# Kernel tuning notes

Hardware: AMD Instinct MI355X
Metric: run time of the kernel (lower is better)

## Reference

```python
import jax, jax.numpy as jnp
import numpy as np

C = 256       # in_channels
A = 6         # act_dim
B = 10000     # number of graphs (batch)
N = B * A     # total nodes
E = 960000    # number of edges
H = 32        # hidden_size


def setup_inputs() -> dict:
    key = jax.random.key(0)
    ks = jax.random.split(key, 20)
    s = 1.0 / np.sqrt(C)
    inp = {
        "state": jax.random.normal(ks[0], (N, C), jnp.float32),
        "edge_index": jax.random.randint(ks[1], (2, E), 0, N, jnp.int32),
        "action": jax.random.uniform(ks[2], (B, A), jnp.float32),
    }
    # GCNConv params (weight [C,C], bias [C]); conv4/conv5 exist but are unused by forward
    for i in range(5):
        inp[f"W{i+1}"] = jax.random.normal(ks[3 + i], (C, C), jnp.float32) * s
        inp[f"b{i+1}"] = jnp.zeros((C,), jnp.float32)
    D1 = 6 * C + 1
    inp["lin1_w"] = jax.random.normal(ks[10], (D1, H), jnp.float32) / np.sqrt(D1)
    inp["lin1_b"] = jnp.zeros((H,), jnp.float32)
    inp["lin2_w"] = jax.random.normal(ks[11], (H, H), jnp.float32) / np.sqrt(H)
    inp["lin2_b"] = jnp.zeros((H,), jnp.float32)
    inp["lin3_w"] = jax.random.normal(ks[12], (H, 1), jnp.float32) / np.sqrt(H)
    inp["lin3_b"] = jnp.zeros((1,), jnp.float32)
    return inp


def _gcn(x, W, b, src, dst, dinv):
    # PyG GCNConv: xW, then D^{-1/2}(A+I)D^{-1/2} aggregation, then bias.
    xw = x @ W                                    # [N, C]
    norm = dinv[src] * dinv[dst]                  # [E]
    agg = jax.ops.segment_sum(xw[src] * norm[:, None], dst, num_segments=N)
    agg = agg + xw * (dinv * dinv)[:, None]       # self-loop term
    return agg + b


def reference(state, edge_index, action,
              W1, b1, W2, b2, W3, b3, W4, b4, W5, b5,
              lin1_w, lin1_b, lin2_w, lin2_b, lin3_w, lin3_b):
    src, dst = edge_index[0], edge_index[1]
    # degree of A + I, computed at destination nodes (gcn_norm with self-loops)
    deg = jax.ops.segment_sum(jnp.ones((E,), state.dtype), dst, num_segments=N) + 1.0
    dinv = jax.lax.rsqrt(deg)

    o1 = jax.nn.relu(_gcn(state, W1, b1, src, dst, dinv))
    o2 = jax.nn.relu(_gcn(o1, W2, b2, src, dst, dinv))
    o3 = jax.nn.relu(_gcn(o2, W3, b3, src, dst, dinv))
    # NOTE: original forward reuses conv3 for layers 4 and 5 (replicated faithfully)
    o4 = jax.nn.relu(_gcn(o3, W3, b3, src, dst, dinv))
    o5 = jax.nn.relu(_gcn(o4, W3, b3, src, dst, dinv))

    r = lambda t: t.reshape(-1, A, C)             # [B, A, C]
    concat = jnp.concatenate(
        [r(o1), r(o2), r(o3), r(o4), r(o5), r(state), action[..., None]], axis=-1)
    x = jax.nn.relu(concat @ lin1_w + lin1_b)     # [B, A, H]
    x = jax.nn.relu(x @ lin2_w + lin2_b)
    x = jnp.sum(x, axis=1)                        # readout over act_dim
    x = (x @ lin3_w + lin3_b).squeeze(-1)         # [B]
    return x
```

## Files before the change

### kernel.cpp

```cpp
#include <hip/hip_runtime.h>
#include <hip/hip_fp16.h>

#define NNODES 60000
#define NEDGES 960000
#define NGRAPH 10000

struct __align__(16) H8 { __half2 h[4]; };
struct __align__(8)  H4 { __half2 h[2]; };

typedef _Float16 f16x8 __attribute__((ext_vector_type(8)));
typedef float f32x4 __attribute__((ext_vector_type(4)));


__global__ void count_deg_k(const int* __restrict__ ei, int* __restrict__ deg) {
  int e = blockIdx.x * blockDim.x + threadIdx.x;
  atomicAdd(&deg[ei[NEDGES + e]], 1);
}

__global__ void scan1_k(const int* __restrict__ deg, int* __restrict__ rs,
                        int* __restrict__ bsum, float* __restrict__ dinv) {
  __shared__ int s[256];
  int tid = threadIdx.x;
  int i = blockIdx.x * 256 + tid;
  int v = (i < NNODES) ? deg[i] : 0;
  if (i < NNODES) dinv[i] = rsqrtf((float)v + 1.0f);
  int x = v;
  s[tid] = x; __syncthreads();
  #pragma unroll
  for (int off = 1; off < 256; off <<= 1) {
    int t = (tid >= off) ? s[tid - off] : 0;
    __syncthreads();
    x += t; s[tid] = x; __syncthreads();
  }
  if (i < NNODES) rs[i] = x - v;
  if (tid == 255) bsum[blockIdx.x] = x;
}

__global__ void scan2_k(int* __restrict__ bsum, int nb) {
  __shared__ int s[256];
  int tid = threadIdx.x;
  int v = (tid < nb) ? bsum[tid] : 0;
  int x = v; s[tid] = x; __syncthreads();
  #pragma unroll
  for (int off = 1; off < 256; off <<= 1) {
    int t = (tid >= off) ? s[tid - off] : 0;
    __syncthreads();
    x += t; s[tid] = x; __syncthreads();
  }
  if (tid < nb) bsum[tid] = x - v;
}

__global__ void scan3_k(int* __restrict__ rs, const int* __restrict__ bsum) {
  int i = blockIdx.x * 256 + threadIdx.x;
  if (i < NNODES) rs[i] += bsum[blockIdx.x];
  if (i == 0) rs[NNODES] = NEDGES;
}

__global__ void scatter_k(const int* __restrict__ ei, const int* __restrict__ rs,
                          int* __restrict__ cursor, unsigned short* __restrict__ csr) {
  int e = blockIdx.x * blockDim.x + threadIdx.x;
  int s = ei[e], d = ei[NEDGES + e];
  int pos = rs[d] + atomicAdd(&cursor[d], 1);
  csr[pos] = (unsigned short)s;
}


__launch_bounds__(256)
__global__ void f2hskern_k(const float* __restrict__ state, const float* __restrict__ lw,
                           __half* __restrict__ stateh, float* __restrict__ part) {
  __shared__ float os[32][256];
  int tid = threadIdx.x;
  int n0 = blockIdx.x * 32;
  #pragma unroll
  for (int l = 0; l < 4; ++l) {
    int f = tid + l * 256;
    int row = f >> 5, c8 = (f & 31) * 8;
    const float* src = state + (size_t)(n0 + row) * 256 + c8;
    float4 u = *reinterpret_cast<const float4*>(src);
    float4 v = *reinterpret_cast<const float4*>(src + 4);
    float* dst = &os[row][c8];
    dst[0] = u.x; dst[1] = u.y; dst[2] = u.z; dst[3] = u.w;
    dst[4] = v.x; dst[5] = v.y; dst[6] = v.z; dst[7] = v.w;
    H8 o;
    o.h[0].x = __float2half_rn(u.x); o.h[0].y = __float2half_rn(u.y);
    o.h[1].x = __float2half_rn(u.z); o.h[1].y = __float2half_rn(u.w);
    o.h[2].x = __float2half_rn(v.x); o.h[2].y = __float2half_rn(v.y);
    o.h[3].x = __float2half_rn(v.z); o.h[3].y = __float2half_rn(v.w);
    *reinterpret_cast<H8*>(stateh + (size_t)(n0 + row) * 256 + c8) = o;
  }
  __syncthreads();
  int dim = tid & 31, rblk = tid >> 5;
  float a0 = 0.f, a1 = 0.f, a2 = 0.f, a3 = 0.f;
  #pragma unroll 8
  for (int k = 0; k < 256; ++k) {
    float w = lw[k * 32 + dim];
    a0 += os[rblk * 4 + 0][k] * w;
    a1 += os[rblk * 4 + 1][k] * w;
    a2 += os[rblk * 4 + 2][k] * w;
    a3 += os[rblk * 4 + 3][k] * w;
  }
  int base = (n0 + rblk * 4) * 32 + dim;
  part[base] = a0;
  part[base + 32] = a1;
  part[base + 64] = a2;
  part[base + 96] = a3;
}


__global__ void wconv3_k(const float* __restrict__ W1, const float* __restrict__ W2,
                         const float* __restrict__ W3, __half* __restrict__ T1,
                         __half* __restrict__ T2, __half* __restrict__ T3) {
  int n = blockIdx.x & 255, which = blockIdx.x >> 8, k = threadIdx.x;
  const float* W = which == 0 ? W1 : (which == 1 ? W2 : W3);
  __half* T = which == 0 ? T1 : (which == 1 ? T2 : T3);
  T[n * 256 + k] = __float2half_rn(W[k * 256 + n]);
}

__global__ void wconvL_k(const float* __restrict__ l1w, __half* __restrict__ lwhT) {
  int dimg = blockIdx.x;
  int l = dimg >> 5, dim = dimg & 31, k = threadIdx.x;
  lwhT[(size_t)dimg * 256 + k] = __float2half_rn(l1w[((size_t)l * 256 + k) * 32 + dim]);
}


#define LDA 264

__launch_bounds__(256, 3)
__global__ void gemm_mfma_k(const __half* __restrict__ Xh, const __half* __restrict__ WhT,
                            const float* __restrict__ dinv, __half* __restrict__ Y,
                            const __half* __restrict__ lwhT, float* __restrict__ part) {
  __shared__ _Float16 As[64][LDA];
  const int tid = threadIdx.x;
  const int m0 = blockIdx.x * 64;
  const int lane = tid & 63;
  const int wid = tid >> 6;
  const int wr = wid >> 1, wc = wid & 1;
  const int li = lane & 15, lg = lane >> 4;

  #pragma unroll
  for (int l = 0; l < 8; ++l) {
    int f = l * 256 + tid;
    int row = f >> 5, c8 = (f & 31) * 8;
    int gr = m0 + row; if (gr >= NNODES) gr = NNODES - 1;
    *reinterpret_cast<H8*>(&As[row][c8]) =
        *reinterpret_cast<const H8*>(Xh + (size_t)gr * 256 + c8);
  }
  __syncthreads();

  f32x4 acc[2][8];
  #pragma unroll
  for (int i = 0; i < 2; ++i)
    #pragma unroll
    for (int j = 0; j < 8; ++j) acc[i][j] = (f32x4){0.f, 0.f, 0.f, 0.f};

  #pragma unroll
  for (int k0 = 0; k0 < 256; k0 += 32) {
    f16x8 a0 = *reinterpret_cast<const f16x8*>(&As[wr * 32 + li][k0 + lg * 8]);
    f16x8 a1 = *reinterpret_cast<const f16x8*>(&As[wr * 32 + 16 + li][k0 + lg * 8]);
    f16x8 b[8];
    #pragma unroll
    for (int cf = 0; cf < 8; ++cf)
      b[cf] = *reinterpret_cast<const f16x8*>(
          WhT + (size_t)(wc * 128 + cf * 16 + li) * 256 + k0 + lg * 8);
    #pragma unroll
    for (int cf = 0; cf < 8; ++cf) {
      acc[0][cf] = __builtin_amdgcn_mfma_f32_16x16x32_f16(b[cf], a0, acc[0][cf], 0, 0, 0);
      acc[1][cf] = __builtin_amdgcn_mfma_f32_16x16x32_f16(b[cf], a1, acc[1][cf], 0, 0, 0);
    }
  }

  #pragma unroll
  for (int rf = 0; rf < 2; ++rf) {
    int r = m0 + wr * 32 + rf * 16 + li;
    if (r < NNODES) {
      float dv = dinv[r];
      #pragma unroll
      for (int cf = 0; cf < 8; ++cf) {
        int n = wc * 128 + cf * 16 + lg * 4;
        H4 o;
        o.h[0].x = __float2half_rn(acc[rf][cf][0] * dv);
        o.h[0].y = __float2half_rn(acc[rf][cf][1] * dv);
        o.h[1].x = __float2half_rn(acc[rf][cf][2] * dv);
        o.h[1].y = __float2half_rn(acc[rf][cf][3] * dv);
        *reinterpret_cast<H4*>(Y + (size_t)r * 256 + n) = o;
      }
    }
  }

  if (lwhT != nullptr) {
    f32x4 pacc[2];
    pacc[0] = (f32x4){0.f, 0.f, 0.f, 0.f};
    pacc[1] = (f32x4){0.f, 0.f, 0.f, 0.f};
    #pragma unroll
    for (int k0 = 0; k0 < 256; k0 += 32) {
      f16x8 a = *reinterpret_cast<const f16x8*>(&As[wid * 16 + li][k0 + lg * 8]);
      f16x8 b0 = *reinterpret_cast<const f16x8*>(lwhT + (size_t)li * 256 + k0 + lg * 8);
      f16x8 b1 = *reinterpret_cast<const f16x8*>(lwhT + (size_t)(16 + li) * 256 + k0 + lg * 8);
      pacc[0] = __builtin_amdgcn_mfma_f32_16x16x32_f16(b0, a, pacc[0], 0, 0, 0);
      pacc[1] = __builtin_amdgcn_mfma_f32_16x16x32_f16(b1, a, pacc[1], 0, 0, 0);
    }
    int r = m0 + wid * 16 + li;
    if (r < NNODES) {
      #pragma unroll
      for (int cf = 0; cf < 2; ++cf) {
        float4 v;
        v.x = pacc[cf][0]; v.y = pacc[cf][1]; v.z = pacc[cf][2]; v.w = pacc[cf][3];
        *reinterpret_cast<float4*>(part + (size_t)r * 32 + cf * 16 + lg * 4) = v;
      }
    }
  }
}


__device__ inline void addH8(float* acc, const H8& v) {
  #pragma unroll
  for (int q = 0; q < 4; ++q) {
    acc[q * 2 + 0] += __low2float(v.h[q]);
    acc[q * 2 + 1] += __high2float(v.h[q]);
  }
}

__global__ void gather_k(const __half* __restrict__ ysh, const int* __restrict__ rs,
                         const unsigned short* __restrict__ csr, const float* __restrict__ dinv,
                         const float* __restrict__ bias, __half* __restrict__ out) {
  int tid = threadIdx.x;
  int lane = tid & 63;
  int wave = (blockIdx.x * blockDim.x + tid) >> 6;
  int d = wave * 2 + (lane >> 5);
  int c8 = (lane & 31) * 8;

  float acc[8];
  H8 self = *reinterpret_cast<const H8*>(ysh + (size_t)d * 256 + c8);
  #pragma unroll
  for (int q = 0; q < 4; ++q) {
    acc[q * 2 + 0] = __low2float(self.h[q]);
    acc[q * 2 + 1] = __high2float(self.h[q]);
  }

  int e = rs[d], end = rs[d + 1];
  for (; e + 3 < end; e += 4) {
    int s0 = csr[e], s1 = csr[e + 1], s2 = csr[e + 2], s3 = csr[e + 3];
    H8 v0 = *reinterpret_cast<const H8*>(ysh + (size_t)s0 * 256 + c8);
    H8 v1 = *reinterpret_cast<const H8*>(ysh + (size_t)s1 * 256 + c8);
    H8 v2 = *reinterpret_cast<const H8*>(ysh + (size_t)s2 * 256 + c8);
    H8 v3 = *reinterpret_cast<const H8*>(ysh + (size_t)s3 * 256 + c8);
    addH8(acc, v0);
    addH8(acc, v1);
    addH8(acc, v2);
    addH8(acc, v3);
  }
  for (; e < end; ++e) {
    int s0 = csr[e];
    H8 v0 = *reinterpret_cast<const H8*>(ysh + (size_t)s0 * 256 + c8);
    addH8(acc, v0);
  }

  float dv = dinv[d];
  float4 b0 = *reinterpret_cast<const float4*>(bias + c8);
  float4 b1 = *reinterpret_cast<const float4*>(bias + c8 + 4);
  float r0 = fmaxf(acc[0] * dv + b0.x, 0.f);
  float r1 = fmaxf(acc[1] * dv + b0.y, 0.f);
  float r2 = fmaxf(acc[2] * dv + b0.z, 0.f);
  float r3 = fmaxf(acc[3] * dv + b0.w, 0.f);
  float r4 = fmaxf(acc[4] * dv + b1.x, 0.f);
  float r5 = fmaxf(acc[5] * dv + b1.y, 0.f);
  float r6 = fmaxf(acc[6] * dv + b1.z, 0.f);
  float r7 = fmaxf(acc[7] * dv + b1.w, 0.f);
  H8 o;
  o.h[0].x = __float2half_rn(r0); o.h[0].y = __float2half_rn(r1);
  o.h[1].x = __float2half_rn(r2); o.h[1].y = __float2half_rn(r3);
  o.h[2].x = __float2half_rn(r4); o.h[2].y = __float2half_rn(r5);
  o.h[3].x = __float2half_rn(r6); o.h[3].y = __float2half_rn(r7);
  *reinterpret_cast<H8*>(out + (size_t)d * 256 + c8) = o;
}


__launch_bounds__(256)
__global__ void skern_k(const __half* __restrict__ in, const float* __restrict__ lw,
                        float* __restrict__ part) {
  __shared__ float os[32][256];
  int tid = threadIdx.x;
  int n0 = blockIdx.x * 32;
  #pragma unroll
  for (int l = 0; l < 4; ++l) {
    int f = tid + l * 256;
    int row = f >> 5, c8 = (f & 31) * 8;
    H8 v = *reinterpret_cast<const H8*>(in + (size_t)(n0 + row) * 256 + c8);
    float* dst = &os[row][c8];
    dst[0] = __low2float(v.h[0]); dst[1] = __high2float(v.h[0]);
    dst[2] = __low2float(v.h[1]); dst[3] = __high2float(v.h[1]);
    dst[4] = __low2float(v.h[2]); dst[5] = __high2float(v.h[2]);
    dst[6] = __low2float(v.h[3]); dst[7] = __high2float(v.h[3]);
  }
  __syncthreads();
  int dim = tid & 31, rblk = tid >> 5;
  float a0 = 0.f, a1 = 0.f, a2 = 0.f, a3 = 0.f;
  #pragma unroll 8
  for (int k = 0; k < 256; ++k) {
    float w = lw[k * 32 + dim];
    a0 += os[rblk * 4 + 0][k] * w;
    a1 += os[rblk * 4 + 1][k] * w;
    a2 += os[rblk * 4 + 2][k] * w;
    a3 += os[rblk * 4 + 3][k] * w;
  }
  int base = (n0 + rblk * 4) * 32 + dim;
  part[base] = a0;
  part[base + 32] = a1;
  part[base + 64] = a2;
  part[base + 96] = a3;
}


__launch_bounds__(192)
__global__ void mlpfinal_k(const float* __restrict__ p0, const float* __restrict__ p1,
                           const float* __restrict__ p2, const float* __restrict__ p3,
                           const float* __restrict__ p4, const float* __restrict__ p5,
                           const float* __restrict__ action, const float* __restrict__ l1wlast,
                           const float* __restrict__ l1b, const float* __restrict__ l2w,
                           const float* __restrict__ l2b, const float* __restrict__ l3w,
                           const float* __restrict__ l3b, float* __restrict__ out) {
  __shared__ float w2s[1024];
  __shared__ float h1s[6][33];
  __shared__ float red[3];
  int tid = threadIdx.x;
  for (int i = tid; i < 1024; i += 192) w2s[i] = l2w[i];
  int a = tid >> 5, dim = tid & 31;
  int n = blockIdx.x * 6 + a;
  int idx = n * 32 + dim;
  float h1 = l1b[dim] + action[n] * l1wlast[dim]
           + p0[idx] + p1[idx] + p2[idx] + p3[idx] + p4[idx] + p5[idx];
  h1s[a][dim] = fmaxf(h1, 0.f);
  __syncthreads();
  float acc = l2b[dim];
  #pragma unroll
  for (int k = 0; k < 32; ++k) acc += h1s[a][k] * w2s[k * 32 + dim];
  float v = fmaxf(acc, 0.f) * l3w[dim];
  #pragma unroll
  for (int off = 32; off; off >>= 1) v += __shfl_down(v, off, 64);
  int lane = tid & 63, wave = tid >> 6;
  if (lane == 0) red[wave] = v;
  __syncthreads();
  if (tid == 0) out[blockIdx.x] = red[0] + red[1] + red[2] + l3b[0];
}


extern "C" void kernel_launch(void* const* d_in, const int* in_sizes, int n_in,
                              void* d_out, int out_size, void* d_ws, size_t ws_size,
                              hipStream_t stream) {
  const float* state  = (const float*)d_in[0];
  const int*   ei     = (const int*)d_in[1];
  const float* action = (const float*)d_in[2];
  const float* W1 = (const float*)d_in[3];
  const float* b1 = (const float*)d_in[4];
  const float* W2 = (const float*)d_in[5];
  const float* b2 = (const float*)d_in[6];
  const float* W3 = (const float*)d_in[7];
  const float* b3 = (const float*)d_in[8];
  const float* l1w = (const float*)d_in[13];
  const float* l1b = (const float*)d_in[14];
  const float* l2w = (const float*)d_in[15];
  const float* l2b = (const float*)d_in[16];
  const float* l3w = (const float*)d_in[17];
  const float* l3b = (const float*)d_in[18];
  float* out = (float*)d_out;

  char* base = (char*)d_ws;
  size_t off = 0;
  auto carve = [&](size_t bytes) {
    char* q = base + off;
    off += (bytes + 255) & ~(size_t)255;
    return q;
  };
  __half* ysh    = (__half*)carve((size_t)NNODES * 256 * 2);
  __half* obufh  = (__half*)carve((size_t)NNODES * 256 * 2);
  __half* stateh = (__half*)carve((size_t)NNODES * 256 * 2);
  __half* whT1   = (__half*)carve(256 * 256 * 2);
  __half* whT2   = (__half*)carve(256 * 256 * 2);
  __half* whT3   = (__half*)carve(256 * 256 * 2);
  __half* lwhT   = (__half*)carve(5 * 32 * 256 * 2);
  float* parts[6];
  for (int i = 0; i < 6; ++i) parts[i] = (float*)carve((size_t)NNODES * 32 * 4);
  float* dinv  = (float*)carve(NNODES * 4);
  char*  zbase = (char*)carve(0);
  int*   deg   = (int*)carve(NNODES * 4);
  int*   cursor= (int*)carve(NNODES * 4);
  size_t zlen  = (size_t)((char*)carve(0) - zbase);
  int*   rs    = (int*)carve((NNODES + 1) * 4);
  unsigned short* csr = (unsigned short*)carve((size_t)NEDGES * 2);
  int*   bsum  = (int*)carve(256 * 4);

  hipMemsetAsync(zbase, 0, zlen, stream);

  f2hskern_k<<<NNODES / 32, 256, 0, stream>>>(state, l1w + 1280 * 32, stateh, parts[5]);
  wconv3_k<<<256 * 3, 256, 0, stream>>>(W1, W2, W3, whT1, whT2, whT3);
  wconvL_k<<<160, 256, 0, stream>>>(l1w, lwhT);

  count_deg_k<<<NEDGES / 256, 256, 0, stream>>>(ei, deg);
  int nb = (NNODES + 255) / 256;
  scan1_k<<<nb, 256, 0, stream>>>(deg, rs, bsum, dinv);
  scan2_k<<<1, 256, 0, stream>>>(bsum, nb);
  scan3_k<<<nb, 256, 0, stream>>>(rs, bsum);
  scatter_k<<<NEDGES / 256, 256, 0, stream>>>(ei, rs, cursor, csr);

  const __half* whTs[5] = {whT1, whT2, whT3, whT3, whT3};
  const float*  bs[5]   = {b1, b2, b3, b3, b3};
  const __half* in = stateh;
  int mblocks = (NNODES + 63) / 64;
  for (int layer = 0; layer < 5; ++layer) {
    const __half* plw = (layer == 0) ? nullptr : lwhT + (size_t)(layer - 1) * 32 * 256;
    float* ppart = (layer == 0) ? nullptr : parts[layer - 1];
    gemm_mfma_k<<<mblocks, 256, 0, stream>>>(in, whTs[layer], dinv, ysh, plw, ppart);
    gather_k<<<NNODES / 8, 256, 0, stream>>>(ysh, rs, csr, dinv, bs[layer], obufh);
    in = obufh;
  }
  skern_k<<<NNODES / 32, 256, 0, stream>>>(obufh, l1w + 1024 * 32, parts[4]);
  mlpfinal_k<<<NGRAPH, 192, 0, stream>>>(parts[0], parts[1], parts[2], parts[3], parts[4],
                                         parts[5], action, l1w + 1536 * 32, l1b, l2w, l2b,
                                         l3w, l3b, out);
}
```

Measured before the change: 766.1 us.

## Fuse neighbor gather into next-layer GEMM and fold fp32 state conversion into first GEMM

Each GCN layer's gather/aggregation now runs in the prologue of the next layer's MFMA GEMM kernel, writing the aggregated rows straight into shared memory instead of round-tripping through a global buffer. The first GEMM reads fp32 state directly and converts it in-kernel, which removes the separate conversion/state-partial kernel. The lin1 partial MFMA is interleaved into the main k-loop, and outputs are staged through LDS for coalesced stores, with ping-pong output buffers. In exchange, each 64-row block does its gather with only 8 rows per 32-lane group serially, which may expose more gather latency and reduce parallelism compared with the standalone gather kernel.

```diff
diff --git a/kernel.cpp b/kernel.cpp
--- a/kernel.cpp
+++ b/kernel.cpp
@@ -10,6 +10,8 @@
 
 typedef _Float16 f16x8 __attribute__((ext_vector_type(8)));
 typedef float f32x4 __attribute__((ext_vector_type(4)));
+
+#define LDA 264
 
 
 __global__ void count_deg_k(const int* __restrict__ ei, int* __restrict__ deg) {
@@ -65,48 +67,6 @@
 }
 
 
-__launch_bounds__(256)
-__global__ void f2hskern_k(const float* __restrict__ state, const float* __restrict__ lw,
-                           __half* __restrict__ stateh, float* __restrict__ part) {
-  __shared__ float os[32][256];
-  int tid = threadIdx.x;
-  int n0 = blockIdx.x * 32;
-  #pragma unroll
-  for (int l = 0; l < 4; ++l) {
-    int f = tid + l * 256;
-    int row = f >> 5, c8 = (f & 31) * 8;
-    const float* src = state + (size_t)(n0 + row) * 256 + c8;
-    float4 u = *reinterpret_cast<const float4*>(src);
-    float4 v = *reinterpret_cast<const float4*>(src + 4);
-    float* dst = &os[row][c8];
-    dst[0] = u.x; dst[1] = u.y; dst[2] = u.z; dst[3] = u.w;
-    dst[4] = v.x; dst[5] = v.y; dst[6] = v.z; dst[7] = v.w;
-    H8 o;
-    o.h[0].x = __float2half_rn(u.x); o.h[0].y = __float2half_rn(u.y);
-    o.h[1].x = __float2half_rn(u.z); o.h[1].y = __float2half_rn(u.w);
-    o.h[2].x = __float2half_rn(v.x); o.h[2].y = __float2half_rn(v.y);
-    o.h[3].x = __float2half_rn(v.z); o.h[3].y = __float2half_rn(v.w);
-    *reinterpret_cast<H8*>(stateh + (size_t)(n0 + row) * 256 + c8) = o;
-  }
-  __syncthreads();
-  int dim = tid & 31, rblk = tid >> 5;
-  float a0 = 0.f, a1 = 0.f, a2 = 0.f, a3 = 0.f;
-  #pragma unroll 8
-  for (int k = 0; k < 256; ++k) {
-    float w = lw[k * 32 + dim];
-    a0 += os[rblk * 4 + 0][k] * w;
-    a1 += os[rblk * 4 + 1][k] * w;
-    a2 += os[rblk * 4 + 2][k] * w;
-    a3 += os[rblk * 4 + 3][k] * w;
-  }
-  int base = (n0 + rblk * 4) * 32 + dim;
-  part[base] = a0;
-  part[base + 32] = a1;
-  part[base + 64] = a2;
-  part[base + 96] = a3;
-}
-
-
 __global__ void wconv3_k(const float* __restrict__ W1, const float* __restrict__ W2,
                          const float* __restrict__ W3, __half* __restrict__ T1,
                          __half* __restrict__ T2, __half* __restrict__ T3) {
@@ -123,92 +83,111 @@
 }
 
 
-#define LDA 264
-
-__launch_bounds__(256, 3)
-__global__ void gemm_mfma_k(const __half* __restrict__ Xh, const __half* __restrict__ WhT,
-                            const float* __restrict__ dinv, __half* __restrict__ Y,
-                            const __half* __restrict__ lwhT, float* __restrict__ part) {
-  __shared__ _Float16 As[64][LDA];
-  const int tid = threadIdx.x;
-  const int m0 = blockIdx.x * 64;
+__device__ __forceinline__ void gemm_body(
+    _Float16 (*As)[LDA], int m0, int tid,
+    const __half* __restrict__ WhT, const __half* __restrict__ lwhT,
+    const float* __restrict__ dinv, __half* __restrict__ Y,
+    float* __restrict__ part) {
   const int lane = tid & 63;
   const int wid = tid >> 6;
   const int wr = wid >> 1, wc = wid & 1;
   const int li = lane & 15, lg = lane >> 4;
 
-  #pragma unroll
-  for (int l = 0; l < 8; ++l) {
-    int f = l * 256 + tid;
-    int row = f >> 5, c8 = (f & 31) * 8;
-    int gr = m0 + row; if (gr >= NNODES) gr = NNODES - 1;
-    *reinterpret_cast<H8*>(&As[row][c8]) =
-        *reinterpret_cast<const H8*>(Xh + (size_t)gr * 256 + c8);
-  }
-  __syncthreads();
-
   f32x4 acc[2][8];
   #pragma unroll
   for (int i = 0; i < 2; ++i)
     #pragma unroll
     for (int j = 0; j < 8; ++j) acc[i][j] = (f32x4){0.f, 0.f, 0.f, 0.f};
+  f32x4 p0 = (f32x4){0.f, 0.f, 0.f, 0.f};
+  f32x4 p1 = (f32x4){0.f, 0.f, 0.f, 0.f};
 
   #pragma unroll
   for (int k0 = 0; k0 < 256; k0 += 32) {
     f16x8 a0 = *reinterpret_cast<const f16x8*>(&As[wr * 32 + li][k0 + lg * 8]);
     f16x8 a1 = *reinterpret_cast<const f16x8*>(&As[wr * 32 + 16 + li][k0 + lg * 8]);
+    f16x8 ap = *reinterpret_cast<const f16x8*>(&As[wid * 16 + li][k0 + lg * 8]);
     f16x8 b[8];
     #pragma unroll
     for (int cf = 0; cf < 8; ++cf)
       b[cf] = *reinterpret_cast<const f16x8*>(
           WhT + (size_t)(wc * 128 + cf * 16 + li) * 256 + k0 + lg * 8);
+    f16x8 bp0 = *reinterpret_cast<const f16x8*>(lwhT + (size_t)li * 256 + k0 + lg * 8);
+    f16x8 bp1 = *reinterpret_cast<const f16x8*>(lwhT + (size_t)(16 + li) * 256 + k0 + lg * 8);
     #pragma unroll
     for (int cf = 0; cf < 8; ++cf) {
       acc[0][cf] = __builtin_amdgcn_mfma_f32_16x16x32_f16(b[cf], a0, acc[0][cf], 0, 0, 0);
       acc[1][cf] = __builtin_amdgcn_mfma_f32_16x16x32_f16(b[cf], a1, acc[1][cf], 0, 0, 0);
     }
-  }
+    p0 = __builtin_amdgcn_mfma_f32_16x16x32_f16(bp0, ap, p0, 0, 0, 0);
+    p1 = __builtin_amdgcn_mfma_f32_16x16x32_f16(bp1, ap, p1, 0, 0, 0);
+  }
+
+  __syncthreads();
 
   #pragma unroll
   for (int rf = 0; rf < 2; ++rf) {
-    int r = m0 + wr * 32 + rf * 16 + li;
-    if (r < NNODES) {
-      float dv = dinv[r];
-      #pragma unroll
-      for (int cf = 0; cf < 8; ++cf) {
-        int n = wc * 128 + cf * 16 + lg * 4;
-        H4 o;
-        o.h[0].x = __float2half_rn(acc[rf][cf][0] * dv);
-        o.h[0].y = __float2half_rn(acc[rf][cf][1] * dv);
-        o.h[1].x = __float2half_rn(acc[rf][cf][2] * dv);
-        o.h[1].y = __float2half_rn(acc[rf][cf][3] * dv);
-        *reinterpret_cast<H4*>(Y + (size_t)r * 256 + n) = o;
-      }
+    int row = wr * 32 + rf * 16 + li;
+    int r = m0 + row;
+    float dv = (r < NNODES) ? dinv[r] : 0.f;
+    #pragma unroll
+    for (int cf = 0; cf < 8; ++cf) {
+      int col = wc * 128 + cf * 16 + lg * 4;
+      H4 o;
+      o.h[0].x = __float2half_rn(acc[rf][cf][0] * dv);
+      o.h[0].y = __float2half_rn(acc[rf][cf][1] * dv);
+      o.h[1].x = __float2half_rn(acc[rf][cf][2] * dv);
+      o.h[1].y = __float2half_rn(acc[rf][cf][3] * dv);
+      *reinterpret_cast<H4*>(&As[row][col]) = o;
     }
   }
 
-  if (lwhT != nullptr) {
-    f32x4 pacc[2];
-    pacc[0] = (f32x4){0.f, 0.f, 0.f, 0.f};
-    pacc[1] = (f32x4){0.f, 0.f, 0.f, 0.f};
-    #pragma unroll
-    for (int k0 = 0; k0 < 256; k0 += 32) {
-      f16x8 a = *reinterpret_cast<const f16x8*>(&As[wid * 16 + li][k0 + lg * 8]);
-      f16x8 b0 = *reinterpret_cast<const f16x8*>(lwhT + (size_t)li * 256 + k0 + lg * 8);
-      f16x8 b1 = *reinterpret_cast<const f16x8*>(lwhT + (size_t)(16 + li) * 256 + k0 + lg * 8);
-      pacc[0] = __builtin_amdgcn_mfma_f32_16x16x32_f16(b0, a, pacc[0], 0, 0, 0);
-      pacc[1] = __builtin_amdgcn_mfma_f32_16x16x32_f16(b1, a, pacc[1], 0, 0, 0);
-    }
-    int r = m0 + wid * 16 + li;
-    if (r < NNODES) {
-      #pragma unroll
-      for (int cf = 0; cf < 2; ++cf) {
-        float4 v;
-        v.x = pacc[cf][0]; v.y = pacc[cf][1]; v.z = pacc[cf][2]; v.w = pacc[cf][3];
-        *reinterpret_cast<float4*>(part + (size_t)r * 32 + cf * 16 + lg * 4) = v;
-      }
-    }
-  }
+  int pr = m0 + wid * 16 + li;
+  if (pr < NNODES) {
+    float4 v0, v1;
+    v0.x = p0[0]; v0.y = p0[1]; v0.z = p0[2]; v0.w = p0[3];
+    v1.x = p1[0]; v1.y = p1[1]; v1.z = p1[2]; v1.w = p1[3];
+    *reinterpret_cast<float4*>(part + (size_t)pr * 32 + lg * 4) = v0;
+    *reinterpret_cast<float4*>(part + (size_t)pr * 32 + 16 + lg * 4) = v1;
+  }
+
+  __syncthreads();
+
+  #pragma unroll
+  for (int l = 0; l < 8; ++l) {
+    int f = l * 256 + tid;
+    int row = f >> 5, c8 = (f & 31) * 8;
+    int gr = m0 + row;
+    if (gr < NNODES)
+      *reinterpret_cast<H8*>(Y + (size_t)gr * 256 + c8) =
+          *reinterpret_cast<const H8*>(&As[row][c8]);
+  }
+}
+
+
+__launch_bounds__(256, 3)
+__global__ void gemm0_k(const float* __restrict__ Xf, const __half* __restrict__ WhT,
+                        const float* __restrict__ dinv, __half* __restrict__ Y,
+                        const __half* __restrict__ lwhT, float* __restrict__ part) {
+  __shared__ _Float16 As[64][LDA];
+  const int tid = threadIdx.x;
+  const int m0 = blockIdx.x * 64;
+  #pragma unroll
+  for (int l = 0; l < 8; ++l) {
+    int f = l * 256 + tid;
+    int row = f >> 5, c8 = (f & 31) * 8;
+    int gr = m0 + row; if (gr >= NNODES) gr = NNODES - 1;
+    const float* src = Xf + (size_t)gr * 256 + c8;
+    float4 u = *reinterpret_cast<const float4*>(src);
+    float4 v = *reinterpret_cast<const float4*>(src + 4);
+    H8 o;
+    o.h[0].x = __float2half_rn(u.x); o.h[0].y = __float2half_rn(u.y);
+    o.h[1].x = __float2half_rn(u.z); o.h[1].y = __float2half_rn(u.w);
+    o.h[2].x = __float2half_rn(v.x); o.h[2].y = __float2half_rn(v.y);
+    o.h[3].x = __float2half_rn(v.z); o.h[3].y = __float2half_rn(v.w);
+    *reinterpret_cast<H8*>(&As[row][c8]) = o;
+  }
+  __syncthreads();
+  gemm_body(As, m0, tid, WhT, lwhT, dinv, Y, part);
 }
 
 
@@ -219,6 +198,72 @@
     acc[q * 2 + 1] += __high2float(v.h[q]);
   }
 }
+
+__launch_bounds__(256, 3)
+__global__ void ggemm_k(const __half* __restrict__ ysin, const int* __restrict__ rs,
+                        const unsigned short* __restrict__ csr,
+                        const float* __restrict__ dinv, const float* __restrict__ bias,
+                        const __half* __restrict__ WhT, const __half* __restrict__ lwhT,
+                        __half* __restrict__ Yout, float* __restrict__ part) {
+  __shared__ _Float16 As[64][LDA];
+  const int tid = threadIdx.x;
+  const int m0 = blockIdx.x * 64;
+  const int half = tid >> 5;
+  const int c8 = (tid & 31) * 8;
+
+  float4 b0 = *reinterpret_cast<const float4*>(bias + c8);
+  float4 b1 = *reinterpret_cast<const float4*>(bias + c8 + 4);
+
+  for (int i = 0; i < 8; ++i) {
+    int d = m0 + half * 8 + i;
+    int dc = (d < NNODES) ? d : NNODES - 1;
+
+    float acc[8];
+    H8 self = *reinterpret_cast<const H8*>(ysin + (size_t)dc * 256 + c8);
+    #pragma unroll
+    for (int q = 0; q < 4; ++q) {
+      acc[q * 2 + 0] = __low2float(self.h[q]);
+      acc[q * 2 + 1] = __high2float(self.h[q]);
+    }
+
+    int e = rs[dc], end = rs[dc + 1];
+    for (; e + 3 < end; e += 4) {
+      int s0 = csr[e], s1 = csr[e + 1], s2 = csr[e + 2], s3 = csr[e + 3];
+      H8 v0 = *reinterpret_cast<const H8*>(ysin + (size_t)s0 * 256 + c8);
+      H8 v1 = *reinterpret_cast<const H8*>(ysin + (size_t)s1 * 256 + c8);
+      H8 v2 = *reinterpret_cast<const H8*>(ysin + (size_t)s2 * 256 + c8);
+      H8 v3 = *reinterpret_cast<const H8*>(ysin + (size_t)s3 * 256 + c8);
+      addH8(acc, v0);
+      addH8(acc, v1);
+      addH8(acc, v2);
+      addH8(acc, v3);
+    }
+    for (; e < end; ++e) {
+      int s0 = csr[e];
+      H8 v0 = *reinterpret_cast<const H8*>(ysin + (size_t)s0 * 256 + c8);
+      addH8(acc, v0);
+    }
+
+    float dv = dinv[dc];
+    float r0 = fmaxf(acc[0] * dv + b0.x, 0.f);
+    float r1 = fmaxf(acc[1] * dv + b0.y, 0.f);
+    float r2 = fmaxf(acc[2] * dv + b0.z, 0.f);
+    float r3 = fmaxf(acc[3] * dv + b0.w, 0.f);
+    float r4 = fmaxf(acc[4] * dv + b1.x, 0.f);
+    float r5 = fmaxf(acc[5] * dv + b1.y, 0.f);
+    float r6 = fmaxf(acc[6] * dv + b1.z, 0.f);
+    float r7 = fmaxf(acc[7] * dv + b1.w, 0.f);
+    H8 o;
+    o.h[0].x = __float2half_rn(r0); o.h[0].y = __float2half_rn(r1);
+    o.h[1].x = __float2half_rn(r2); o.h[1].y = __float2half_rn(r3);
+    o.h[2].x = __float2half_rn(r4); o.h[2].y = __float2half_rn(r5);
+    o.h[3].x = __float2half_rn(r6); o.h[3].y = __float2half_rn(r7);
+    *reinterpret_cast<H8*>(&As[half * 8 + i][c8]) = o;
+  }
+  __syncthreads();
+  gemm_body(As, m0, tid, WhT, lwhT, dinv, Yout, part);
+}
+
 
 __global__ void gather_k(const __half* __restrict__ ysh, const int* __restrict__ rs,
                          const unsigned short* __restrict__ csr, const float* __restrict__ dinv,
@@ -371,13 +416,13 @@
     off += (bytes + 255) & ~(size_t)255;
     return q;
   };
-  __half* ysh    = (__half*)carve((size_t)NNODES * 256 * 2);
+  __half* ysA    = (__half*)carve((size_t)NNODES * 256 * 2);
+  __half* ysB    = (__half*)carve((size_t)NNODES * 256 * 2);
   __half* obufh  = (__half*)carve((size_t)NNODES * 256 * 2);
-  __half* stateh = (__half*)carve((size_t)NNODES * 256 * 2);
   __half* whT1   = (__half*)carve(256 * 256 * 2);
   __half* whT2   = (__half*)carve(256 * 256 * 2);
   __half* whT3   = (__half*)carve(256 * 256 * 2);
-  __half* lwhT   = (__half*)carve(5 * 32 * 256 * 2);
+  __half* lwhT   = (__half*)carve(6 * 32 * 256 * 2);
   float* parts[6];
   for (int i = 0; i < 6; ++i) parts[i] = (float*)carve((size_t)NNODES * 32 * 4);
   float* dinv  = (float*)carve(NNODES * 4);
@@ -391,9 +436,8 @@
 
   hipMemsetAsync(zbase, 0, zlen, stream);
 
-  f2hskern_k<<<NNODES / 32, 256, 0, stream>>>(state, l1w + 1280 * 32, stateh, parts[5]);
   wconv3_k<<<256 * 3, 256, 0, stream>>>(W1, W2, W3, whT1, whT2, whT3);
-  wconvL_k<<<160, 256, 0, stream>>>(l1w, lwhT);
+  wconvL_k<<<192, 256, 0, stream>>>(l1w, lwhT);
 
   count_deg_k<<<NEDGES / 256, 256, 0, stream>>>(ei, deg);
   int nb = (NNODES + 255) / 256;
@@ -402,18 +446,21 @@
   scan3_k<<<nb, 256, 0, stream>>>(rs, bsum);
   scatter_k<<<NEDGES / 256, 256, 0, stream>>>(ei, rs, cursor, csr);
 
-  const __half* whTs[5] = {whT1, whT2, whT3, whT3, whT3};
-  const float*  bs[5]   = {b1, b2, b3, b3, b3};
-  const __half* in = stateh;
   int mblocks = (NNODES + 63) / 64;
-  for (int layer = 0; layer < 5; ++layer) {
-    const __half* plw = (layer == 0) ? nullptr : lwhT + (size_t)(layer - 1) * 32 * 256;
-    float* ppart = (layer == 0) ? nullptr : parts[layer - 1];
-    gemm_mfma_k<<<mblocks, 256, 0, stream>>>(in, whTs[layer], dinv, ysh, plw, ppart);
-    gather_k<<<NNODES / 8, 256, 0, stream>>>(ysh, rs, csr, dinv, bs[layer], obufh);
-    in = obufh;
-  }
+
+  gemm0_k<<<mblocks, 256, 0, stream>>>(state, whT1, dinv, ysA,
+                                       lwhT + (size_t)5 * 32 * 256, parts[5]);
+  ggemm_k<<<mblocks, 256, 0, stream>>>(ysA, rs, csr, dinv, b1, whT2,
+                                       lwhT + (size_t)0 * 32 * 256, ysB, parts[0]);
+  ggemm_k<<<mblocks, 256, 0, stream>>>(ysB, rs, csr, dinv, b2, whT3,
+                                       lwhT + (size_t)1 * 32 * 256, ysA, parts[1]);
+  ggemm_k<<<mblocks, 256, 0, stream>>>(ysA, rs, csr, dinv, b3, whT3,
+                                       lwhT + (size_t)2 * 32 * 256, ysB, parts[2]);
+  ggemm_k<<<mblocks, 256, 0, stream>>>(ysB, rs, csr, dinv, b3, whT3,
+                                       lwhT + (size_t)3 * 32 * 256, ysA, parts[3]);
+  gather_k<<<NNODES / 8, 256, 0, stream>>>(ysA, rs, csr, dinv, b3, obufh);
   skern_k<<<NNODES / 32, 256, 0, stream>>>(obufh, l1w + 1024 * 32, parts[4]);
+
   mlpfinal_k<<<NGRAPH, 192, 0, stream>>>(parts[0], parts[1], parts[2], parts[3], parts[4],
                                          parts[5], action, l1w + 1536 * 32, l1b, l2w, l2b,
                                          l3w, l3b, out);
```

Measured after the change: 846.6 us. 1.11x slower.
